# Kernel optimization log

Hardware: AMD Instinct MI355X
Metric: run time of the kernel (lower is better)

## Reference

```python
import jax, jax.numpy as jnp
import numpy as np
import math

B, H, S, D = 2, 12, 2048, 64

def setup_inputs() -> dict:
    key = jax.random.key(0)
    kq, kk, kv, km = jax.random.split(key, 4)
    Q = jax.random.normal(kq, (B, H, S, D), dtype=jnp.float32)
    K = jax.random.normal(kk, (B, H, S, D), dtype=jnp.float32)
    V = jax.random.normal(kv, (B, H, S, D), dtype=jnp.float32)
    mask = jax.random.randint(km, (B, 1, S, S), 0, 2, dtype=jnp.int32)
    return {"Q": Q, "K": K, "V": V, "mask": mask}

def reference(Q, K, V, mask):
    d_k = K.shape[-1]
    # [B,H,S,S] scores
    scores = jnp.einsum('bhqd,bhkd->bhqk', Q, K) / math.sqrt(d_k)
    scores = jnp.where(mask == 0, jnp.float32(-1e20), scores)
    attn = jax.nn.softmax(scores, axis=-1)
    # dropout p=0 -> identity
    return jnp.einsum('bhqk,bhkd->bhqd', attn, V)
```

## Files before the change

### kernel.cpp

```cpp
#include <hip/hip_runtime.h>
#include <hip/hip_bf16.h>
#include <math.h>


#define BB 2
#define HH 12
#define SS 2048
#define DD 64
#define BQ 128
#define BK 64
#define GG 4
#define KG (SS / GG)
#define NTG (KG / BK)
#define LT 76
#define NROWS (BB * HH * SS)
#define QSCALE 0.1803368801111f

typedef __attribute__((ext_vector_type(8))) short bf8_t;
typedef __attribute__((ext_vector_type(4))) short bf4_t;
typedef __attribute__((ext_vector_type(4))) float f4_t;
typedef __attribute__((ext_vector_type(4))) unsigned u4_t;
typedef unsigned long long u64;

__device__ __forceinline__ short f2bf(float f) {
    __hip_bfloat16 h = __float2bfloat16(f);
    return *reinterpret_cast<short*>(&h);
}

__device__ __forceinline__ void gl_lds16(const void* g, void* l) {
    __builtin_amdgcn_global_load_lds(
        (const __attribute__((address_space(1))) unsigned*)(g),
        (__attribute__((address_space(3))) unsigned*)(l), 16, 0, 0);
}

__device__ __forceinline__ bf8_t ldfrag(const unsigned short* buf, int row, int c8) {
    return *(const bf8_t*)&buf[((row << 3) | (c8 ^ (row & 7))) << 3];
}
__device__ __forceinline__ bf4_t ldfrag64(const unsigned short* buf, int row,
                                          int c8, int half8) {
    return *(const bf4_t*)&buf[((((row << 3) | (c8 ^ (row & 7))) << 3)) + half8 * 4];
}

__global__ __launch_bounds__(256) void prepass(
    const float* __restrict__ V, const float* __restrict__ K,
    const int* __restrict__ M, unsigned short* __restrict__ Vt,
    unsigned short* __restrict__ Kb, u64* __restrict__ Mbt)
{
    __shared__ unsigned short Ts[64][LT];
    const int bx   = blockIdx.x;
    const int tid  = threadIdx.x;
    const int w    = tid >> 6;
    const int lane = tid & 63;
    const int b    = bx >> 11;
    const int row  = bx & 2047;

    {
        const int* src = M + (size_t)bx * SS;
        #pragma unroll
        for (int p = 0; p < 8; ++p) {
            int k = p * 256 + w * 64 + lane;
            u64 bm = __ballot(src[k] != 0);
            if (lane == 0)
                Mbt[(size_t)b * 32 * SS + (size_t)(p * 4 + w) * SS + row] = bm;
        }
    }

    if (bx < 768) {
        const int s0 = (bx & 31) * 64;
        const int bh = bx >> 5;
        const float* Vg = V + (size_t)bh * SS * DD;
        #pragma unroll
        for (int pass = 0; pass < 4; ++pass) {
            int c = tid + pass * 256;
            int r = c >> 4, col = (c & 15) * 4;
            float4 v = *(const float4*)(Vg + (size_t)(s0 + r) * DD + col);
            bf4_t p; p.x = f2bf(v.x); p.y = f2bf(v.y); p.z = f2bf(v.z); p.w = f2bf(v.w);
            *(bf4_t*)&Ts[r][col] = p;
        }
        __syncthreads();
        unsigned short* Vo = Vt + (size_t)bh * DD * SS;
        #pragma unroll
        for (int pass = 0; pass < 2; ++pass) {
            int c = tid + pass * 256;
            int d = c >> 3, sc = (c & 7) * 8;
            unsigned short t[8];
            #pragma unroll
            for (int u = 0; u < 8; ++u) t[u] = Ts[sc + u][d];
            uint4 o;
            o.x = (unsigned)t[0] | ((unsigned)t[1] << 16);
            o.y = (unsigned)t[2] | ((unsigned)t[3] << 16);
            o.z = (unsigned)t[4] | ((unsigned)t[5] << 16);
            o.w = (unsigned)t[6] | ((unsigned)t[7] << 16);
            *(uint4*)(Vo + (size_t)d * SS + s0 + sc) = o;
        }
    } else if (bx < 2304) {
        size_t i = ((size_t)(bx - 768) * 256 + tid) * 8;
        float4 a = *(const float4*)(K + i);
        float4 b2 = *(const float4*)(K + i + 4);
        uint4 o;
        o.x = (unsigned short)f2bf(a.x)  | ((unsigned)(unsigned short)f2bf(a.y)  << 16);
        o.y = (unsigned short)f2bf(a.z)  | ((unsigned)(unsigned short)f2bf(a.w)  << 16);
        o.z = (unsigned short)f2bf(b2.x) | ((unsigned)(unsigned short)f2bf(b2.y) << 16);
        o.w = (unsigned short)f2bf(b2.z) | ((unsigned)(unsigned short)f2bf(b2.w) << 16);
        *(uint4*)(Kb + i) = o;
    }
}

__global__ __launch_bounds__(256, 4) void attn_fwd(
    const float* __restrict__ Q, const unsigned short* __restrict__ Kb,
    const unsigned short* __restrict__ Vt, const u64* __restrict__ Mbt,
    float* __restrict__ Opart, float* __restrict__ Lpart)
{
    __shared__ unsigned short Ks[2 * BK * DD];
    __shared__ unsigned short Vts[2 * BK * DD];

    const int tid  = threadIdx.x;
    const int w    = tid >> 6;
    const int lane = tid & 63;
    const int quad = lane >> 4;
    const int l16  = lane & 15;
    const int q0   = blockIdx.x * BQ;
    const int bh   = blockIdx.y;
    const int g    = blockIdx.z;
    const int b    = bh / HH;
    const int qbase = w * 32;

    const float*          Qg = Q  + (size_t)bh * SS * DD;
    const unsigned short* Kg = Kb + (size_t)bh * SS * DD;
    const unsigned short* Vg = Vt + (size_t)bh * DD * SS;
    float* Og = Opart + ((size_t)g * BB * HH + bh) * SS * DD;
    float* Lg = Lpart + (size_t)g * NROWS + (size_t)bh * SS;

    bf8_t bq[2][2];
    #pragma unroll
    for (int qf = 0; qf < 2; ++qf)
        #pragma unroll
        for (int ks = 0; ks < 2; ++ks) {
            const float* qp = Qg + (size_t)(q0 + qbase + qf * 16 + l16) * DD
                                 + ks * 32 + quad * 8;
            float4 x = *(const float4*)qp;
            float4 y = *(const float4*)(qp + 4);
            bf8_t f;
            f[0] = f2bf(x.x * QSCALE); f[1] = f2bf(x.y * QSCALE);
            f[2] = f2bf(x.z * QSCALE); f[3] = f2bf(x.w * QSCALE);
            f[4] = f2bf(y.x * QSCALE); f[5] = f2bf(y.y * QSCALE);
            f[6] = f2bf(y.z * QSCALE); f[7] = f2bf(y.w * QSCALE);
            bq[qf][ks] = f;
        }

    bf8_t onesf;
    {
        short ov = (l16 == 0) ? (short)0x3F80 : (short)0;
        #pragma unroll
        for (int j = 0; j < 8; ++j) onesf[j] = ov;
    }

    f4_t oacc[2][4], lacc[2];
    #pragma unroll
    for (int qf = 0; qf < 2; ++qf) {
        lacc[qf] = (f4_t){0.f, 0.f, 0.f, 0.f};
        #pragma unroll
        for (int nf = 0; nf < 4; ++nf) oacc[qf][nf] = (f4_t){0.f, 0.f, 0.f, 0.f};
    }

    const unsigned short* kSrc[2];
    const unsigned short* vSrc[2];
    unsigned short*       kDst[2];
    unsigned short*       vDst[2];
    #pragma unroll
    for (int j = 0; j < 2; ++j) {
        const int bc = (w * 2 + j) * 64;
        const int c  = bc + lane;
        const int r  = c >> 3;
        const int c8 = (c & 7) ^ (r & 7);
        kSrc[j] = Kg + (size_t)(g * KG + r) * DD + c8 * 8;
        vSrc[j] = Vg + (size_t)r * SS + g * KG + c8 * 8;
        kDst[j] = Ks  + bc * 8;
        vDst[j] = Vts + bc * 8;
    }
    const u64* mp[2];
    u64 mpf[2];
    #pragma unroll
    for (int qf = 0; qf < 2; ++qf) {
        mp[qf] = Mbt + (size_t)b * 32 * SS + (size_t)(g * NTG) * SS
                     + q0 + qbase + qf * 16 + l16;
        mpf[qf] = *mp[qf];
    }

    #pragma unroll
    for (int j = 0; j < 2; ++j) {
        gl_lds16(kSrc[j], kDst[j]);
        gl_lds16(vSrc[j], vDst[j]);
        kSrc[j] += BK * DD;
        vSrc[j] += BK;
    }
    __syncthreads();

    for (int t = 0; t < NTG; ++t) {
        const int cb = (t & 1) * (BK * DD);
        if (t + 1 < NTG) {
            const int nb = ((t + 1) & 1) * (BK * DD);
            #pragma unroll
            for (int j = 0; j < 2; ++j) {
                gl_lds16(kSrc[j], kDst[j] + nb);
                gl_lds16(vSrc[j], vDst[j] + nb);
                kSrc[j] += BK * DD;
                vSrc[j] += BK;
            }
        }
        const u64 cm[2] = {mpf[0] >> (quad * 4), mpf[1] >> (quad * 4)};
        if (t + 1 < NTG) {
            #pragma unroll
            for (int qf = 0; qf < 2; ++qf) {
                mp[qf] += SS;
                mpf[qf] = *mp[qf];
            }
        }
        const unsigned short* Kst = Ks  + cb;
        const unsigned short* Vst = Vts + cb;

        #pragma unroll
        for (int h = 0; h < 2; ++h) {
            unsigned aw[2][4];
            #pragma unroll
            for (int kfh = 0; kfh < 2; ++kfh) {
                const int kf = h * 2 + kfh;
                bf8_t ak0 = ldfrag(Kst, kf * 16 + l16, quad);
                bf8_t ak1 = ldfrag(Kst, kf * 16 + l16, 4 + quad);
                #pragma unroll
                for (int qf = 0; qf < 2; ++qf) {
                    f4_t s = (f4_t){0.f, 0.f, 0.f, 0.f};
                    s = __builtin_amdgcn_mfma_f32_16x16x32_bf16(ak0, bq[qf][0], s, 0, 0, 0);
                    s = __builtin_amdgcn_mfma_f32_16x16x32_bf16(ak1, bq[qf][1], s, 0, 0, 0);
                    float e[4];
                    #pragma unroll
                    for (int r = 0; r < 4; ++r) {
                        float v = __builtin_amdgcn_exp2f(s[r]);
                        e[r] = ((cm[qf] >> (kf * 16 + r)) & 1ull) ? v : 0.f;
                    }
                    aw[qf][kfh * 2 + 0] = __builtin_amdgcn_perm(
                        __float_as_uint(e[1]), __float_as_uint(e[0]), 0x07060302u);
                    aw[qf][kfh * 2 + 1] = __builtin_amdgcn_perm(
                        __float_as_uint(e[3]), __float_as_uint(e[2]), 0x07060302u);
                }
            }
            bf8_t ap[2];
            #pragma unroll
            for (int qf = 0; qf < 2; ++qf) {
                u4_t wds = (u4_t){aw[qf][0], aw[qf][1], aw[qf][2], aw[qf][3]};
                ap[qf] = __builtin_bit_cast(bf8_t, wds);
                lacc[qf] = __builtin_amdgcn_mfma_f32_16x16x32_bf16(
                    ap[qf], onesf, lacc[qf], 0, 0, 0);
            }
            #pragma unroll
            for (int nf = 0; nf < 4; ++nf) {
                bf4_t lo = ldfrag64(Vst, nf * 16 + l16, h * 4 + (quad >> 1), quad & 1);
                bf4_t hi = ldfrag64(Vst, nf * 16 + l16, h * 4 + 2 + (quad >> 1), quad & 1);
                bf8_t bv = __builtin_shufflevector(lo, hi, 0, 1, 2, 3, 4, 5, 6, 7);
                #pragma unroll
                for (int qf = 0; qf < 2; ++qf)
                    oacc[qf][nf] = __builtin_amdgcn_mfma_f32_16x16x32_bf16(
                        ap[qf], bv, oacc[qf][nf], 0, 0, 0);
            }
        }
        if (t + 1 < NTG) __syncthreads();
    }

    #pragma unroll
    for (int qf = 0; qf < 2; ++qf) {
        #pragma unroll
        for (int r = 0; r < 4; ++r) {
            const int row = q0 + qbase + qf * 16 + quad * 4 + r;
            #pragma unroll
            for (int nf = 0; nf < 4; ++nf)
                Og[(size_t)row * DD + nf * 16 + l16] = oacc[qf][nf][r];
        }
        if (l16 == 0) {
            #pragma unroll
            for (int r = 0; r < 4; ++r)
                Lg[q0 + qbase + qf * 16 + quad * 4 + r] = lacc[qf][r];
        }
    }
}

__global__ __launch_bounds__(256) void reduce_o(
    const float* __restrict__ Opart, const float* __restrict__ Lpart,
    float* __restrict__ O)
{
    const size_t idx = (size_t)blockIdx.x * 256 + threadIdx.x;
    const size_t row = idx >> 4;
    const int    c   = (int)(idx & 15) * 4;
    float4 acc = {0.f, 0.f, 0.f, 0.f};
    float  l   = 0.f;
    #pragma unroll
    for (int g = 0; g < GG; ++g) {
        float4 a = *(const float4*)(Opart + ((size_t)g * NROWS + row) * DD + c);
        acc.x += a.x; acc.y += a.y; acc.z += a.z; acc.w += a.w;
        l += Lpart[(size_t)g * NROWS + row];
    }
    const float inv = 1.f / l;
    float4 o;
    o.x = acc.x * inv; o.y = acc.y * inv; o.z = acc.z * inv; o.w = acc.w * inv;
    *(float4*)(O + row * DD + c) = o;
}

extern "C" void kernel_launch(void* const* d_in, const int* in_sizes, int n_in,
                              void* d_out, int out_size, void* d_ws, size_t ws_size,
                              hipStream_t stream) {
    const float* Q = (const float*)d_in[0];
    const float* K = (const float*)d_in[1];
    const float* V = (const float*)d_in[2];
    const int*   M = (const int*)d_in[3];
    float*       O = (float*)d_out;

    unsigned short* Vt    = (unsigned short*)d_ws;
    unsigned short* Kb    = Vt + (size_t)BB * HH * SS * DD;
    u64*            Mbt   = (u64*)(Kb + (size_t)BB * HH * SS * DD);
    float*          Opart = (float*)(Mbt + (size_t)BB * 32 * SS);
    float*          Lpart = Opart + (size_t)GG * NROWS * DD;

    prepass<<<dim3(BB * SS), 256, 0, stream>>>(V, K, M, Vt, Kb, Mbt);
    attn_fwd<<<dim3(SS / BQ, BB * HH, GG), 256, 0, stream>>>(Q, Kb, Vt, Mbt,
                                                             Opart, Lpart);
    reduce_o<<<dim3((NROWS * DD / 4) / 256), 256, 0, stream>>>(Opart, Lpart, O);
}
```

Before: 157.2 us.

## Fuse split-K reduction into attention kernel via atomic last-block fixup

Removes the separate reduce_o launch. Each attention block now bumps a per-tile atomic counter (zeroed in the prepass), and the last of the GG split blocks sums the partial O and L and writes the normalized output. Separately, the V transpose store reorders rows so the PV B-fragment loads as one 16-byte swizzled ldfrag instead of two 8-byte halves plus a shuffle. The goal is to save one launch and one pass over the partials, at the cost of an atomic, fences and a serialized tail on the last block.

```diff
diff --git a/kernel.cpp b/kernel.cpp
--- a/kernel.cpp
+++ b/kernel.cpp
@@ -12,6 +12,8 @@
 #define GG 4
 #define KG (SS / GG)
 #define NTG (KG / BK)
+#define NQB (SS / BQ)
+#define NCNT (NQB * BB * HH)
 #define LT 76
 #define NROWS (BB * HH * SS)
 #define QSCALE 0.1803368801111f
@@ -36,15 +38,12 @@
 __device__ __forceinline__ bf8_t ldfrag(const unsigned short* buf, int row, int c8) {
     return *(const bf8_t*)&buf[((row << 3) | (c8 ^ (row & 7))) << 3];
 }
-__device__ __forceinline__ bf4_t ldfrag64(const unsigned short* buf, int row,
-                                          int c8, int half8) {
-    return *(const bf4_t*)&buf[((((row << 3) | (c8 ^ (row & 7))) << 3)) + half8 * 4];
-}
 
 __global__ __launch_bounds__(256) void prepass(
     const float* __restrict__ V, const float* __restrict__ K,
     const int* __restrict__ M, unsigned short* __restrict__ Vt,
-    unsigned short* __restrict__ Kb, u64* __restrict__ Mbt)
+    unsigned short* __restrict__ Kb, u64* __restrict__ Mbt,
+    unsigned* __restrict__ Cnt)
 {
     __shared__ unsigned short Ts[64][LT];
     const int bx   = blockIdx.x;
@@ -54,6 +53,8 @@
     const int b    = bx >> 11;
     const int row  = bx & 2047;
 
+    if (tid == 0 && bx < NCNT) Cnt[bx] = 0;
+
     {
         const int* src = M + (size_t)bx * SS;
         #pragma unroll
@@ -83,9 +84,13 @@
         for (int pass = 0; pass < 2; ++pass) {
             int c = tid + pass * 256;
             int d = c >> 3, sc = (c & 7) * 8;
+            const int hh32 = sc & 32;
+            const int qq4  = (sc >> 1) & 12;
             unsigned short t[8];
             #pragma unroll
-            for (int u = 0; u < 8; ++u) t[u] = Ts[sc + u][d];
+            for (int u = 0; u < 4; ++u) t[u]     = Ts[hh32 + qq4 + u][d];
+            #pragma unroll
+            for (int u = 0; u < 4; ++u) t[4 + u] = Ts[hh32 + 16 + qq4 + u][d];
             uint4 o;
             o.x = (unsigned)t[0] | ((unsigned)t[1] << 16);
             o.y = (unsigned)t[2] | ((unsigned)t[3] << 16);
@@ -109,10 +114,12 @@
 __global__ __launch_bounds__(256, 4) void attn_fwd(
     const float* __restrict__ Q, const unsigned short* __restrict__ Kb,
     const unsigned short* __restrict__ Vt, const u64* __restrict__ Mbt,
-    float* __restrict__ Opart, float* __restrict__ Lpart)
+    float* __restrict__ Opart, float* __restrict__ Lpart,
+    float* __restrict__ O, unsigned* __restrict__ Cnt)
 {
     __shared__ unsigned short Ks[2 * BK * DD];
     __shared__ unsigned short Vts[2 * BK * DD];
+    __shared__ unsigned fixup_last;
 
     const int tid  = threadIdx.x;
     const int w    = tid >> 6;
@@ -254,9 +261,7 @@
             }
             #pragma unroll
             for (int nf = 0; nf < 4; ++nf) {
-                bf4_t lo = ldfrag64(Vst, nf * 16 + l16, h * 4 + (quad >> 1), quad & 1);
-                bf4_t hi = ldfrag64(Vst, nf * 16 + l16, h * 4 + 2 + (quad >> 1), quad & 1);
-                bf8_t bv = __builtin_shufflevector(lo, hi, 0, 1, 2, 3, 4, 5, 6, 7);
+                bf8_t bv = ldfrag(Vst, nf * 16 + l16, h * 4 + quad);
                 #pragma unroll
                 for (int qf = 0; qf < 2; ++qf)
                     oacc[qf][nf] = __builtin_amdgcn_mfma_f32_16x16x32_bf16(
@@ -281,27 +286,39 @@
                 Lg[q0 + qbase + qf * 16 + quad * 4 + r] = lacc[qf][r];
         }
     }
-}
-
-__global__ __launch_bounds__(256) void reduce_o(
-    const float* __restrict__ Opart, const float* __restrict__ Lpart,
-    float* __restrict__ O)
-{
-    const size_t idx = (size_t)blockIdx.x * 256 + threadIdx.x;
-    const size_t row = idx >> 4;
-    const int    c   = (int)(idx & 15) * 4;
-    float4 acc = {0.f, 0.f, 0.f, 0.f};
-    float  l   = 0.f;
-    #pragma unroll
-    for (int g = 0; g < GG; ++g) {
-        float4 a = *(const float4*)(Opart + ((size_t)g * NROWS + row) * DD + c);
-        acc.x += a.x; acc.y += a.y; acc.z += a.z; acc.w += a.w;
-        l += Lpart[(size_t)g * NROWS + row];
-    }
-    const float inv = 1.f / l;
-    float4 o;
-    o.x = acc.x * inv; o.y = acc.y * inv; o.z = acc.z * inv; o.w = acc.w * inv;
-    *(float4*)(O + row * DD + c) = o;
+
+    __syncthreads();
+    if (tid == 0) {
+        __threadfence();
+        unsigned old = atomicAdd(&Cnt[(unsigned)bh * NQB + blockIdx.x], 1u);
+        fixup_last = (old == GG - 1) ? 1u : 0u;
+    }
+    __syncthreads();
+    if (fixup_last) {
+        __threadfence();
+        #pragma unroll
+        for (int it = 0; it < 8; ++it) {
+            const int u    = it * 256 + tid;
+            const int row  = u >> 4;
+            const int cc   = (u & 15) * 4;
+            const size_t r4 = (size_t)(q0 + row);
+            float4 acc = {0.f, 0.f, 0.f, 0.f};
+            float  l   = 0.f;
+            #pragma unroll
+            for (int g2 = 0; g2 < GG; ++g2) {
+                const float* op = Opart + ((size_t)g2 * BB * HH + bh) * SS * DD
+                                        + r4 * DD + cc;
+                float4 a = *(const float4*)op;
+                acc.x += a.x; acc.y += a.y; acc.z += a.z; acc.w += a.w;
+                l += Lpart[(size_t)g2 * NROWS + (size_t)bh * SS + r4];
+            }
+            const float inv = 1.f / l;
+            float4 o;
+            o.x = acc.x * inv; o.y = acc.y * inv;
+            o.z = acc.z * inv; o.w = acc.w * inv;
+            *(float4*)(O + ((size_t)bh * SS + r4) * DD + cc) = o;
+        }
+    }
 }
 
 extern "C" void kernel_launch(void* const* d_in, const int* in_sizes, int n_in,
@@ -318,9 +335,9 @@
     u64*            Mbt   = (u64*)(Kb + (size_t)BB * HH * SS * DD);
     float*          Opart = (float*)(Mbt + (size_t)BB * 32 * SS);
     float*          Lpart = Opart + (size_t)GG * NROWS * DD;
-
-    prepass<<<dim3(BB * SS), 256, 0, stream>>>(V, K, M, Vt, Kb, Mbt);
-    attn_fwd<<<dim3(SS / BQ, BB * HH, GG), 256, 0, stream>>>(Q, Kb, Vt, Mbt,
-                                                             Opart, Lpart);
-    reduce_o<<<dim3((NROWS * DD / 4) / 256), 256, 0, stream>>>(Opart, Lpart, O);
-}
+    unsigned*       Cnt   = (unsigned*)(Lpart + (size_t)GG * NROWS);
+
+    prepass<<<dim3(BB * SS), 256, 0, stream>>>(V, K, M, Vt, Kb, Mbt, Cnt);
+    attn_fwd<<<dim3(NQB, BB * HH, GG), 256, 0, stream>>>(Q, Kb, Vt, Mbt,
+                                                         Opart, Lpart, O, Cnt);
+}
```

Measured after the change: 253.3 us. +61.2%, slower.
